# Performance work log

Measured on AMD Instinct MI355X. Metric: run time of the kernel, lower is better.

## Reference

```python
import jax, jax.numpy as jnp
import numpy as np

H, HKV, HD = 16, 4, 128
EPS = 1.1920928955078125e-07  # float32 eps, torch F.rms_norm default


def _rms_norm(t):
    return t * jax.lax.rsqrt(jnp.mean(t * t, axis=-1, keepdims=True) + EPS)


def _rope(t, cos, sin):
    # t: [B, T, h, HD]; cos/sin: [T, HD//2] -> broadcast [1, T, 1, HD//2]
    te, to = t[..., 0::2], t[..., 1::2]
    c = cos[None, :, None, :]
    s = sin[None, :, None, :]
    re = te * c - to * s
    ro = te * s + to * c
    return jnp.stack((re, ro), axis=-1).reshape(t.shape)


def setup_inputs() -> dict:
    key = jax.random.key(0)
    ks = jax.random.split(key, 5)
    B, T, C = 2, 2048, 2048
    return {
        "x": jax.random.normal(ks[0], (B, T, C), jnp.float32),
        "Wq": jax.random.normal(ks[1], (C, C), jnp.float32) * 0.02,
        "Wk": jax.random.normal(ks[2], (HKV * HD, C), jnp.float32) * 0.02,
        "Wv": jax.random.normal(ks[3], (HKV * HD, C), jnp.float32) * 0.02,
        "Wo": jax.random.normal(ks[4], (C, C), jnp.float32) * 0.02,
        "q_gain": jnp.full((H,), 5.0, jnp.float32),
    }


def reference(x, Wq, Wk, Wv, Wo, q_gain):
    B, T, C = x.shape
    q = (x @ Wq.T).reshape(B, T, H, HD)
    k = (x @ Wk.T).reshape(B, T, HKV, HD)
    v = (x @ Wv.T).reshape(B, T, HKV, HD)

    q = _rms_norm(q)
    k = _rms_norm(k)

    theta = 1.0 / (10000.0 ** (jnp.arange(0, HD, 2, dtype=jnp.float32) / HD))
    t = jnp.arange(T, dtype=jnp.float32)
    freqs = jnp.outer(t, theta)  # [T, HD//2]
    cos, sin = jnp.cos(freqs), jnp.sin(freqs)

    q = _rope(q, cos, sin)
    k = _rope(k, cos, sin)
    q = q * q_gain[None, None, :, None]

    qh = q.transpose(0, 2, 1, 3)                       # [B, H, T, HD]
    kh = jnp.repeat(k.transpose(0, 2, 1, 3), H // HKV, axis=1)
    vh = jnp.repeat(v.transpose(0, 2, 1, 3), H // HKV, axis=1)

    scale = 1.0 / jnp.sqrt(jnp.float32(HD))
    scores = jnp.einsum("bhqd,bhkd->bhqk", qh, kh) * scale
    causal = jnp.tril(jnp.ones((T, T), bool))
    scores = jnp.where(causal[None, None], scores, jnp.finfo(scores.dtype).min)
    attn = jax.nn.softmax(scores, axis=-1)
    out = jnp.einsum("bhqk,bhkd->bhqd", attn, vh)
    out = out.transpose(0, 2, 1, 3).reshape(B, T, C)
    return out @ Wo.T
```

## Files before the change

### kernel.cpp

```cpp
#include <hip/hip_runtime.h>
#include <hip/hip_bf16.h>

#define TSEQ 2048
#define CDIM 2048
#define NH   16
#define NKV  4
#define HDIM 128
#define BATCH 2
#define MROWS (BATCH*TSEQ)
#define KVC   (NKV*HDIM)
#define QKVC  (CDIM + 2*KVC)

typedef short bf16x8 __attribute__((ext_vector_type(8)));
typedef float f32x4  __attribute__((ext_vector_type(4)));

typedef const __attribute__((address_space(1))) void* gptr_t;
typedef __attribute__((address_space(3))) void* sptr_t;

__device__ inline void async16(const __hip_bfloat16* g, __hip_bfloat16* l) {
  __builtin_amdgcn_global_load_lds((gptr_t)g, (sptr_t)l, 16, 0, 0);
}

__device__ inline f32x4 mfma16(bf16x8 a, bf16x8 b, f32x4 c) {
  return __builtin_amdgcn_mfma_f32_16x16x32_bf16(a, b, c, 0, 0, 0);
}

__device__ inline float bfbits2f(unsigned short u) {
  return __uint_as_float(((unsigned)u) << 16);
}

__device__ inline int swz128(int row, int col) {
  return row*128 + (((col >> 3) ^ (row & 15)) << 3) + (col & 7);
}
__device__ inline int swz64(int row, int col) {
  return row*64 + ((((col >> 3) ^ row) & 7) << 3) + (col & 7);
}

__global__ void canary(const void* __restrict__ x, int* __restrict__ flag) {
  __shared__ int cnt[256];
  int tid = threadIdx.x;
  const unsigned short* u = (const unsigned short*)x;
  int c = 0;
#pragma unroll
  for (int i = 0; i < 4; ++i) {
    float a = fabsf(bfbits2f(u[(tid*4 + i)*2]));
    if (a >= 1e-6f && a <= 1e3f) c++;
  }
  cnt[tid] = c;
  __syncthreads();
  for (int s = 128; s > 0; s >>= 1) {
    if (tid < s) cnt[tid] += cnt[tid + s];
    __syncthreads();
  }
  if (tid == 0) *flag = (cnt[0] > 512) ? 1 : 0;
}

__global__ __launch_bounds__(256) void canonize_all(
    const void* __restrict__ xs,  const void* __restrict__ wqs,
    const void* __restrict__ wks, const void* __restrict__ wvs,
    const void* __restrict__ wos, const void* __restrict__ gs,
    __hip_bfloat16* __restrict__ xd,
    __hip_bfloat16* __restrict__ wqkv,
    __hip_bfloat16* __restrict__ wod,
    __hip_bfloat16* __restrict__ gd,
    const int* __restrict__ flag)
{
  int blk = blockIdx.x;
  const void* src; __hip_bfloat16* dst; int base, n;
  if      (blk < 4096) { src = xs;  dst = xd;                base = blk;        n = MROWS*CDIM; }
  else if (blk < 6144) { src = wqs; dst = wqkv;              base = blk - 4096; n = CDIM*CDIM; }
  else if (blk < 6656) { src = wks; dst = wqkv + (size_t)CDIM*CDIM;            base = blk - 6144; n = KVC*CDIM; }
  else if (blk < 7168) { src = wvs; dst = wqkv + (size_t)(CDIM+KVC)*CDIM;      base = blk - 6656; n = KVC*CDIM; }
  else if (blk < 9216) { src = wos; dst = wod;               base = blk - 7168; n = CDIM*CDIM; }
  else                 { src = gs;  dst = gd;                base = 0;          n = NH; }
  int idx = base*2048 + threadIdx.x*8;
  if (idx >= n) return;
  if (*flag) {
    *(bf16x8*)&dst[idx] = *(const bf16x8*)((const __hip_bfloat16*)src + idx);
  } else {
    const float* s = (const float*)src + idx;
#pragma unroll
    for (int j = 0; j < 8; ++j) dst[idx + j] = __float2bfloat16(s[j]);
  }
}

#define BK 64

__global__ __launch_bounds__(512, 2) void gemm_bt256(
    const __hip_bfloat16* __restrict__ A,
    const __hip_bfloat16* __restrict__ B,
    __hip_bfloat16* __restrict__ C,
    int M, int N, int K, int lda)
{
  __shared__ __align__(16) __hip_bfloat16 As[2][256*BK];
  __shared__ __align__(16) __hip_bfloat16 Bs[2][256*BK];
  const int tid  = threadIdx.x;
  const int wave = tid >> 6;
  const int lane = tid & 63;
  const int qd   = lane >> 4;
  const int ln   = lane & 15;
  const int m0   = blockIdx.y * 256;
  const int n0   = blockIdx.x * 256;
  const int wm   = (wave >> 2) * 128;
  const int wn   = (wave & 3) * 64;

  auto stageA = [&](int half, int buf, int kt) {
    const __hip_bfloat16* src = A + (size_t)(m0 + half*128)*lda + kt*BK;
    __hip_bfloat16* dst = &As[buf][half*128*BK];
#pragma unroll
    for (int i = 0; i < 2; ++i) {
      int c = i*512 + tid;
      int row = c >> 3, sl = c & 7;
      int gs = sl ^ (row & 7);
      async16(&src[(size_t)row*lda + gs*8], &dst[(i*512 + wave*64)*8]);
    }
  };
  auto stageB = [&](int half, int buf, int kt) {
    const __hip_bfloat16* src = B + (size_t)(n0 + half*128)*K + kt*BK;
    __hip_bfloat16* dst = &Bs[buf][half*128*BK];
#pragma unroll
    for (int i = 0; i < 2; ++i) {
      int c = i*512 + tid;
      int row = c >> 3, sl = c & 7;
      int gs = sl ^ (row & 7);
      async16(&src[(size_t)row*K + gs*8], &dst[(i*512 + wave*64)*8]);
    }
  };
  auto ldA = [&](int buf, int m, int kk) -> bf16x8 {
    int row = wm + m*16 + ln;
    return *(const bf16x8*)&As[buf][row*BK + (((kk*4 + qd) ^ (row & 7)) << 3)];
  };
  auto ldB = [&](int buf, int n, int kk) -> bf16x8 {
    int row = wn + n*16 + ln;
    return *(const bf16x8*)&Bs[buf][row*BK + (((kk*4 + qd) ^ (row & 7)) << 3)];
  };

  f32x4 acc[8][4] = {};
  const int nt = K / BK;

  stageA(0, 0, 0); stageA(1, 0, 0);
  stageB(0, 0, 0); stageB(1, 0, 0);
  if (nt > 1) {
    stageA(0, 1, 1); stageA(1, 1, 1);
    asm volatile("s_waitcnt vmcnt(4)" ::: "memory");
  } else {
    asm volatile("s_waitcnt vmcnt(0)" ::: "memory");
  }
  __builtin_amdgcn_s_barrier();

#pragma unroll 1
  for (int t = 0; t < nt; ++t) {
    const int buf = t & 1;
    bf16x8 a03[4][2], a47[4][2], b01[2][2], b23[2][2];

#pragma unroll
    for (int m = 0; m < 4; ++m)
#pragma unroll
      for (int kk = 0; kk < 2; ++kk) a03[m][kk] = ldA(buf, m, kk);
#pragma unroll
    for (int n = 0; n < 2; ++n)
#pragma unroll
      for (int kk = 0; kk < 2; ++kk) b01[n][kk] = ldB(buf, n, kk);
    if (t + 1 < nt) { stageB(0, buf ^ 1, t + 1); stageB(1, buf ^ 1, t + 1); }
    __builtin_amdgcn_s_setprio(1);
#pragma unroll
    for (int m = 0; m < 4; ++m)
#pragma unroll
      for (int n = 0; n < 2; ++n)
#pragma unroll
        for (int kk = 0; kk < 2; ++kk)
          acc[m][n] = mfma16(a03[m][kk], b01[n][kk], acc[m][n]);
    __builtin_amdgcn_s_setprio(0);
    __builtin_amdgcn_s_barrier();

#pragma unroll
    for (int m = 0; m < 4; ++m)
#pragma unroll
      for (int kk = 0; kk < 2; ++kk) a47[m][kk] = ldA(buf, 4 + m, kk);
    __builtin_amdgcn_s_setprio(1);
#pragma unroll
    for (int m = 0; m < 4; ++m)
#pragma unroll
      for (int n = 0; n < 2; ++n)
#pragma unroll
        for (int kk = 0; kk < 2; ++kk)
          acc[4 + m][n] = mfma16(a47[m][kk], b01[n][kk], acc[4 + m][n]);
    __builtin_amdgcn_s_setprio(0);
    __builtin_amdgcn_s_barrier();

#pragma unroll
    for (int n = 0; n < 2; ++n)
#pragma unroll
      for (int kk = 0; kk < 2; ++kk) b23[n][kk] = ldB(buf, 2 + n, kk);
    __builtin_amdgcn_s_setprio(1);
#pragma unroll
    for (int m = 0; m < 4; ++m)
#pragma unroll
      for (int n = 0; n < 2; ++n)
#pragma unroll
        for (int kk = 0; kk < 2; ++kk)
          acc[m][2 + n] = mfma16(a03[m][kk], b23[n][kk], acc[m][2 + n]);
    __builtin_amdgcn_s_setprio(0);
    __builtin_amdgcn_s_barrier();

    if (t + 2 < nt) { stageA(0, buf, t + 2); stageA(1, buf, t + 2); }
    __builtin_amdgcn_s_setprio(1);
#pragma unroll
    for (int m = 0; m < 4; ++m)
#pragma unroll
      for (int n = 0; n < 2; ++n)
#pragma unroll
        for (int kk = 0; kk < 2; ++kk)
          acc[4 + m][2 + n] = mfma16(a47[m][kk], b23[n][kk], acc[4 + m][2 + n]);
    __builtin_amdgcn_s_setprio(0);
    if (t + 2 < nt) asm volatile("s_waitcnt vmcnt(4)" ::: "memory");
    else            asm volatile("s_waitcnt vmcnt(0)" ::: "memory");
    __builtin_amdgcn_s_barrier();
  }

#pragma unroll
  for (int m = 0; m < 8; ++m)
#pragma unroll
    for (int n = 0; n < 4; ++n) {
      int row = m0 + wm + m*16 + qd*4;
      int col = n0 + wn + n*16 + ln;
#pragma unroll
      for (int r = 0; r < 4; ++r)
        C[(size_t)(row + r)*N + col] = __float2bfloat16(acc[m][n][r]);
    }
}

__global__ __launch_bounds__(256, 2) void gemm_out(
    const __hip_bfloat16* __restrict__ A,
    const __hip_bfloat16* __restrict__ B,
    void* __restrict__ C,
    int M, int N, int K, int lda, const int* __restrict__ flag)
{
  __shared__ __align__(16) __hip_bfloat16 As[128*32];
  __shared__ __align__(16) __hip_bfloat16 Bs[128*32];
  const int tid  = threadIdx.x;
  const int wave = tid >> 6;
  const int lane = tid & 63;
  const int qd   = lane >> 4;
  const int ln   = lane & 15;
  const int m0   = blockIdx.y * 128;
  const int n0   = blockIdx.x * 128;
  const int wm   = (wave >> 1) * 64;
  const int wn   = (wave & 1) * 64;

  f32x4 acc[4][4] = {};

  for (int k0 = 0; k0 < K; k0 += 32) {
    __syncthreads();
#pragma unroll
    for (int r = 0; r < 2; ++r) {
      int e   = (r*256 + tid) * 8;
      int row = e >> 5;
      int col = e & 31;
      async16(&A[(size_t)(m0+row)*lda + k0 + col], &As[(size_t)(r*256 + wave*64)*8]);
      async16(&B[(size_t)(n0+row)*K   + k0 + col], &Bs[(size_t)(r*256 + wave*64)*8]);
    }
    __syncthreads();
    bf16x8 af[4], bfr[4];
#pragma unroll
    for (int i = 0; i < 4; ++i)
      af[i] = *(const bf16x8*)&As[(wm + i*16 + ln)*32 + qd*8];
#pragma unroll
    for (int j = 0; j < 4; ++j)
      bfr[j] = *(const bf16x8*)&Bs[(wn + j*16 + ln)*32 + qd*8];
#pragma unroll
    for (int i = 0; i < 4; ++i)
#pragma unroll
      for (int j = 0; j < 4; ++j)
        acc[i][j] = mfma16(af[i], bfr[j], acc[i][j]);
  }
  const bool isbf = (*flag != 0);
#pragma unroll
  for (int i = 0; i < 4; ++i)
#pragma unroll
    for (int j = 0; j < 4; ++j) {
      int row = m0 + wm + i*16 + qd*4;
      int col = n0 + wn + j*16 + ln;
#pragma unroll
      for (int r = 0; r < 4; ++r) {
        if (isbf) ((__hip_bfloat16*)C)[(size_t)(row + r)*N + col] = __float2bfloat16(acc[i][j][r]);
        else      ((float*)C)[(size_t)(row + r)*N + col] = acc[i][j][r];
      }
    }
}

__global__ __launch_bounds__(256) void prep_qk(
    __hip_bfloat16* __restrict__ qkv,
    const __hip_bfloat16* __restrict__ gain)
{
  int wid  = blockIdx.x * 4 + (threadIdx.x >> 6);
  int lane = threadIdx.x & 63;
  bool isq = wid < MROWS*NH;
  int m, h;
  __hip_bfloat16* p;
  if (isq) { m = wid >> 4; h = wid & 15; p = qkv + (size_t)m*QKVC + h*HDIM; }
  else     { int w2 = wid - MROWS*NH; m = w2 >> 2; h = w2 & 3; p = qkv + (size_t)m*QKVC + CDIM + h*HDIM; }

  ushort2 raw = *(const ushort2*)((const unsigned short*)p + 2*lane);
  float e = bfbits2f(raw.x), o = bfbits2f(raw.y);
  float ss = e*e + o*o;
#pragma unroll
  for (int off = 32; off >= 1; off >>= 1) ss += __shfl_xor(ss, off);
  float rms = rsqrtf(ss * (1.0f/128.0f) + 1.1920928955078125e-07f);
  e *= rms; o *= rms;

  float theta = exp2f(-(float)(2*lane) * (1.0f/128.0f) * 13.287712379549449f);
  int t = m & (TSEQ-1);
  float fr = (float)t * theta;
  float c = cosf(fr), s = sinf(fr);
  float re = e*c - o*s;
  float ro = e*s + o*c;

  if (isq) {
    float g = bfbits2f(*(const unsigned short*)&gain[h]) * 0.08838834764831845f;
    re *= g; ro *= g;
  }
  p[2*lane]   = __float2bfloat16(re);
  p[2*lane+1] = __float2bfloat16(ro);
}

__global__ __launch_bounds__(256) void transpose_v(
    const __hip_bfloat16* __restrict__ qkv, __hip_bfloat16* __restrict__ vt)
{
  __shared__ __hip_bfloat16 tile[32][34];
  int tx = threadIdx.x & 31;
  int ty = threadIdx.x >> 5;
  int r0 = blockIdx.x * 32;
  int c0 = blockIdx.y * 32;
#pragma unroll
  for (int i = 0; i < 4; ++i)
    tile[ty + i*8][tx] = qkv[(size_t)(r0 + ty + i*8)*QKVC + (CDIM + KVC) + c0 + tx];
  __syncthreads();
  int b = r0 >> 11;
  int t = r0 & (TSEQ-1);
  int hk = c0 >> 7;
  int d0 = c0 & (HDIM-1);
#pragma unroll
  for (int i = 0; i < 4; ++i) {
    int d = d0 + ty + i*8;
    vt[((size_t)((b*NKV + hk)*HDIM + d))*TSEQ + t + tx] = tile[tx][ty + i*8];
  }
}

__global__ __launch_bounds__(256, 2) void attn_kernel(
    const __hip_bfloat16* __restrict__ qkv,
    const __hip_bfloat16* __restrict__ vt,
    __hip_bfloat16* __restrict__ out)
{
  const int tid  = threadIdx.x;
  const int wave = tid >> 6;
  const int lane = tid & 63;
  const int qd = lane >> 4, ln = lane & 15;
  const int qt = 15 - blockIdx.x;
  const int h  = blockIdx.y;
  const int b  = blockIdx.z;
  const int hk = h >> 2;

  const __hip_bfloat16* K = qkv + (size_t)(b*TSEQ)*QKVC + CDIM + hk*HDIM;
  const __hip_bfloat16* V = vt + ((size_t)(b*NKV + hk)*HDIM)*TSEQ;

  __shared__ __align__(16) __hip_bfloat16 Ks[64*128];
  __shared__ __align__(16) __hip_bfloat16 Vs[128*64];
  __shared__ __align__(16) __hip_bfloat16 Pb[4*32*64];

  auto issueK = [&](int t0) {
#pragma unroll
    for (int i = 0; i < 4; ++i) {
      int c = i*256 + tid;
      int row = c >> 4, cc = c & 15;
      int gcc = cc ^ (row & 15);
      async16(&K[(size_t)(t0 + row)*QKVC + gcc*8], &Ks[(i*256 + wave*64)*8]);
    }
  };
  auto issueV = [&](int t0) {
#pragma unroll
    for (int i = 0; i < 4; ++i) {
      int c = i*256 + tid;
      int row = c >> 3, cc = c & 7;
      int gcc = cc ^ (row & 7);
      async16(&V[(size_t)row*TSEQ + t0 + gcc*8], &Vs[(i*256 + wave*64)*8]);
    }
  };

  const int q0  = qt * 128;
  const int qws = q0 + wave * 32;

  bf16x8 qfr[2][4];
#pragma unroll
  for (int sub = 0; sub < 2; ++sub)
#pragma unroll
    for (int kc = 0; kc < 4; ++kc)
      qfr[sub][kc] = *(const bf16x8*)&qkv[((size_t)(b*TSEQ + qws + sub*16 + ln))*QKVC + h*HDIM + kc*32 + qd*8];

  f32x4 o[2][8] = {};
  float lacc[2][4] = {};

  issueK(0);
  __syncthreads();

  const int ktend = 2*qt + 1;
#pragma unroll 1
  for (int kt = 0; kt <= ktend; ++kt) {
    const int t0 = kt * 64;
    issueV(t0);

    f32x4 sc[2][4] = {};
#pragma unroll
    for (int nt = 0; nt < 4; ++nt) {
#pragma unroll
      for (int kc = 0; kc < 4; ++kc) {
        bf16x8 kfr = *(const bf16x8*)&Ks[swz128(nt*16 + ln, kc*32 + qd*8)];
        sc[0][nt] = mfma16(qfr[0][kc], kfr, sc[0][nt]);
        sc[1][nt] = mfma16(qfr[1][kc], kfr, sc[1][nt]);
      }
    }
    if (t0 + 63 > qws) {
#pragma unroll
      for (int sub = 0; sub < 2; ++sub)
#pragma unroll
        for (int nt = 0; nt < 4; ++nt)
#pragma unroll
          for (int r = 0; r < 4; ++r) {
            int row = qws + sub*16 + qd*4 + r;
            int col = t0 + nt*16 + ln;
            if (col > row) sc[sub][nt][r] = -1.0e30f;
          }
    }
#pragma unroll
    for (int sub = 0; sub < 2; ++sub) {
#pragma unroll
      for (int nt = 0; nt < 4; ++nt)
#pragma unroll
        for (int r = 0; r < 4; ++r)
          sc[sub][nt][r] = __expf(sc[sub][nt][r]);
#pragma unroll
      for (int r = 0; r < 4; ++r)
        lacc[sub][r] += (sc[sub][0][r] + sc[sub][1][r]) + (sc[sub][2][r] + sc[sub][3][r]);
    }

    __hip_bfloat16* Pw = &Pb[wave*2048];
#pragma unroll
    for (int sub = 0; sub < 2; ++sub)
#pragma unroll
      for (int nt = 0; nt < 4; ++nt)
#pragma unroll
        for (int r = 0; r < 4; ++r)
          Pw[swz64(sub*16 + qd*4 + r, nt*16 + ln)] = __float2bfloat16(sc[sub][nt][r]);
    bf16x8 pa[2][2];
#pragma unroll
    for (int sub = 0; sub < 2; ++sub)
#pragma unroll
      for (int kc = 0; kc < 2; ++kc)
        pa[sub][kc] = *(const bf16x8*)&Pw[swz64(sub*16 + ln, kc*32 + qd*8)];

    __syncthreads();
    if (kt < ktend) issueK(t0 + 64);

#pragma unroll
    for (int dt = 0; dt < 8; ++dt) {
#pragma unroll
      for (int kc = 0; kc < 2; ++kc) {
        bf16x8 vf = *(const bf16x8*)&Vs[swz64(dt*16 + ln, kc*32 + qd*8)];
        o[0][dt] = mfma16(pa[0][kc], vf, o[0][dt]);
        o[1][dt] = mfma16(pa[1][kc], vf, o[1][dt]);
      }
    }
    __syncthreads();
  }

  float inv[2][4];
#pragma unroll
  for (int sub = 0; sub < 2; ++sub)
#pragma unroll
    for (int r = 0; r < 4; ++r) {
      float lr = lacc[sub][r];
      lr += __shfl_xor(lr, 1);
      lr += __shfl_xor(lr, 2);
      lr += __shfl_xor(lr, 4);
      lr += __shfl_xor(lr, 8);
      inv[sub][r] = 1.0f / lr;
    }

  __hip_bfloat16* Ow0 = &Ks[wave*2048];
  __hip_bfloat16* Ow1 = &Vs[wave*2048];
#pragma unroll
  for (int dt = 0; dt < 8; ++dt)
#pragma unroll
    for (int r = 0; r < 4; ++r) {
      Ow0[(qd*4 + r)*128 + dt*16 + ln] = __float2bfloat16(o[0][dt][r] * inv[0][r]);
      Ow1[(qd*4 + r)*128 + dt*16 + ln] = __float2bfloat16(o[1][dt][r] * inv[1][r]);
    }
  __syncthreads();
#pragma unroll
  for (int pass = 0; pass < 4; ++pass) {
    int row = pass*4 + qd;
    bf16x8 v0 = *(const bf16x8*)&Ow0[row*128 + ln*8];
    bf16x8 v1 = *(const bf16x8*)&Ow1[row*128 + ln*8];
    int qa = qws + row;
    int qb = qws + 16 + row;
    *(bf16x8*)&out[((size_t)(b*TSEQ + qa))*CDIM + h*HDIM + ln*8] = v0;
    *(bf16x8*)&out[((size_t)(b*TSEQ + qb))*CDIM + h*HDIM + ln*8] = v1;
  }
}

extern "C" void kernel_launch(void* const* d_in, const int* in_sizes, int n_in,
                              void* d_out, int out_size, void* d_ws, size_t ws_size,
                              hipStream_t stream) {
  char* ws = (char*)d_ws;
  size_t off = 0;
  auto alloc = [&](size_t bytes) { char* p = ws + off; off += (bytes + 255) & ~(size_t)255; return p; };

  int* flag = (int*)alloc(256);
  __hip_bfloat16* xb   = (__hip_bfloat16*)alloc((size_t)MROWS*CDIM*2);
  __hip_bfloat16* wqkv = (__hip_bfloat16*)alloc((size_t)QKVC*CDIM*2);
  __hip_bfloat16* wob  = (__hip_bfloat16*)alloc((size_t)CDIM*CDIM*2);
  __hip_bfloat16* gb   = (__hip_bfloat16*)alloc(256);
  __hip_bfloat16* qkv  = (__hip_bfloat16*)alloc((size_t)MROWS*QKVC*2);
  __hip_bfloat16* vt   = (__hip_bfloat16*)alloc((size_t)MROWS*KVC*2);

  canary<<<1, 256, 0, stream>>>(d_in[0], flag);

  canonize_all<<<9217, 256, 0, stream>>>(
      d_in[0], d_in[1], d_in[2], d_in[3], d_in[4], d_in[5],
      xb, wqkv, wob, gb, flag);

  gemm_bt256<<<dim3(QKVC/256, MROWS/256), 512, 0, stream>>>(
      xb, wqkv, qkv, MROWS, QKVC, CDIM, CDIM);

  int nwaves = MROWS*NH + MROWS*NKV;
  prep_qk<<<nwaves/4, 256, 0, stream>>>(qkv, gb);

  transpose_v<<<dim3(MROWS/32, KVC/32), 256, 0, stream>>>(qkv, vt);

  attn_kernel<<<dim3(TSEQ/128, NH, BATCH), 256, 0, stream>>>(qkv, vt, xb);

  gemm_out<<<dim3(CDIM/128, MROWS/128), 256, 0, stream>>>(
      xb, wob, d_out, MROWS, CDIM, CDIM, CDIM, flag);
}
```

Before: 322.3 us.

## Pair light and heavy 64-row query tiles per attention block for causal balance

The attention kernel now runs 128-thread blocks (2 waves) that each process two 64-row query tiles, p and 31-p, one after the other, so every block does the same amount of causal work. Before, each block handled one 128-row tile with 4 waves and the work per block varied widely. The aim is to remove load imbalance and tail effects across the grid. In exchange, each block has fewer waves to hide latency, and the K and V tiles are reloaded separately for each segment.

Result: slower. 348.7 us (+8.2%).

```diff
diff --git a/kernel.cpp b/kernel.cpp
--- a/kernel.cpp
+++ b/kernel.cpp
@@ -347,7 +347,7 @@
   }
 }
 
-__global__ __launch_bounds__(256, 2) void attn_kernel(
+__global__ __launch_bounds__(128, 2) void attn_kernel(
     const __hip_bfloat16* __restrict__ qkv,
     const __hip_bfloat16* __restrict__ vt,
     __hip_bfloat16* __restrict__ out)
@@ -356,7 +356,7 @@
   const int wave = tid >> 6;
   const int lane = tid & 63;
   const int qd = lane >> 4, ln = lane & 15;
-  const int qt = 15 - blockIdx.x;
+  const int p  = blockIdx.x;
   const int h  = blockIdx.y;
   const int b  = blockIdx.z;
   const int hk = h >> 2;
@@ -366,145 +366,145 @@
 
   __shared__ __align__(16) __hip_bfloat16 Ks[64*128];
   __shared__ __align__(16) __hip_bfloat16 Vs[128*64];
-  __shared__ __align__(16) __hip_bfloat16 Pb[4*32*64];
+  __shared__ __align__(16) __hip_bfloat16 Pb[2*32*64];
 
   auto issueK = [&](int t0) {
 #pragma unroll
-    for (int i = 0; i < 4; ++i) {
-      int c = i*256 + tid;
+    for (int i = 0; i < 8; ++i) {
+      int c = i*128 + tid;
       int row = c >> 4, cc = c & 15;
       int gcc = cc ^ (row & 15);
-      async16(&K[(size_t)(t0 + row)*QKVC + gcc*8], &Ks[(i*256 + wave*64)*8]);
+      async16(&K[(size_t)(t0 + row)*QKVC + gcc*8], &Ks[(i*128 + wave*64)*8]);
     }
   };
   auto issueV = [&](int t0) {
 #pragma unroll
-    for (int i = 0; i < 4; ++i) {
-      int c = i*256 + tid;
+    for (int i = 0; i < 8; ++i) {
+      int c = i*128 + tid;
       int row = c >> 3, cc = c & 7;
       int gcc = cc ^ (row & 7);
-      async16(&V[(size_t)row*TSEQ + t0 + gcc*8], &Vs[(i*256 + wave*64)*8]);
+      async16(&V[(size_t)row*TSEQ + t0 + gcc*8], &Vs[(i*128 + wave*64)*8]);
     }
   };
 
-  const int q0  = qt * 128;
-  const int qws = q0 + wave * 32;
-
-  bf16x8 qfr[2][4];
-#pragma unroll
-  for (int sub = 0; sub < 2; ++sub)
-#pragma unroll
-    for (int kc = 0; kc < 4; ++kc)
-      qfr[sub][kc] = *(const bf16x8*)&qkv[((size_t)(b*TSEQ + qws + sub*16 + ln))*QKVC + h*HDIM + kc*32 + qd*8];
-
-  f32x4 o[2][8] = {};
-  float lacc[2][4] = {};
-
-  issueK(0);
-  __syncthreads();
-
-  const int ktend = 2*qt + 1;
 #pragma unroll 1
-  for (int kt = 0; kt <= ktend; ++kt) {
-    const int t0 = kt * 64;
-    issueV(t0);
-
-    f32x4 sc[2][4] = {};
-#pragma unroll
-    for (int nt = 0; nt < 4; ++nt) {
-#pragma unroll
-      for (int kc = 0; kc < 4; ++kc) {
-        bf16x8 kfr = *(const bf16x8*)&Ks[swz128(nt*16 + ln, kc*32 + qd*8)];
-        sc[0][nt] = mfma16(qfr[0][kc], kfr, sc[0][nt]);
-        sc[1][nt] = mfma16(qfr[1][kc], kfr, sc[1][nt]);
+  for (int seg = 0; seg < 2; ++seg) {
+    const int qt = seg ? (31 - p) : p;
+    const int q0 = qt * 64;
+    const int qws = q0 + wave * 32;
+
+    bf16x8 qfr[2][4];
+#pragma unroll
+    for (int sub = 0; sub < 2; ++sub)
+#pragma unroll
+      for (int kc = 0; kc < 4; ++kc)
+        qfr[sub][kc] = *(const bf16x8*)&qkv[((size_t)(b*TSEQ + qws + sub*16 + ln))*QKVC + h*HDIM + kc*32 + qd*8];
+
+    f32x4 o[2][8] = {};
+    float lacc[2][4] = {};
+
+    __syncthreads();
+    issueK(0);
+    __syncthreads();
+
+#pragma unroll 1
+    for (int kt = 0; kt <= qt; ++kt) {
+      const int t0 = kt * 64;
+      issueV(t0);
+
+      f32x4 sc[2][4] = {};
+#pragma unroll
+      for (int nt = 0; nt < 4; ++nt) {
+#pragma unroll
+        for (int kc = 0; kc < 4; ++kc) {
+          bf16x8 kfr = *(const bf16x8*)&Ks[swz128(nt*16 + ln, kc*32 + qd*8)];
+          sc[0][nt] = mfma16(qfr[0][kc], kfr, sc[0][nt]);
+          sc[1][nt] = mfma16(qfr[1][kc], kfr, sc[1][nt]);
+        }
       }
-    }
-    if (t0 + 63 > qws) {
+      if (t0 + 63 > qws) {
+#pragma unroll
+        for (int sub = 0; sub < 2; ++sub)
+#pragma unroll
+          for (int nt = 0; nt < 4; ++nt)
+#pragma unroll
+            for (int r = 0; r < 4; ++r) {
+              int row = qws + sub*16 + qd*4 + r;
+              int col = t0 + nt*16 + ln;
+              if (col > row) sc[sub][nt][r] = -1.0e30f;
+            }
+      }
+#pragma unroll
+      for (int sub = 0; sub < 2; ++sub) {
+#pragma unroll
+        for (int nt = 0; nt < 4; ++nt)
+#pragma unroll
+          for (int r = 0; r < 4; ++r)
+            sc[sub][nt][r] = __expf(sc[sub][nt][r]);
+#pragma unroll
+        for (int r = 0; r < 4; ++r)
+          lacc[sub][r] += (sc[sub][0][r] + sc[sub][1][r]) + (sc[sub][2][r] + sc[sub][3][r]);
+      }
+
+      __hip_bfloat16* Pw = &Pb[wave*2048];
 #pragma unroll
       for (int sub = 0; sub < 2; ++sub)
 #pragma unroll
         for (int nt = 0; nt < 4; ++nt)
 #pragma unroll
-          for (int r = 0; r < 4; ++r) {
-            int row = qws + sub*16 + qd*4 + r;
-            int col = t0 + nt*16 + ln;
-            if (col > row) sc[sub][nt][r] = -1.0e30f;
-          }
-    }
-#pragma unroll
-    for (int sub = 0; sub < 2; ++sub) {
-#pragma unroll
-      for (int nt = 0; nt < 4; ++nt)
+          for (int r = 0; r < 4; ++r)
+            Pw[swz64(sub*16 + qd*4 + r, nt*16 + ln)] = __float2bfloat16(sc[sub][nt][r]);
+      bf16x8 pa[2][2];
+#pragma unroll
+      for (int sub = 0; sub < 2; ++sub)
+#pragma unroll
+        for (int kc = 0; kc < 2; ++kc)
+          pa[sub][kc] = *(const bf16x8*)&Pw[swz64(sub*16 + ln, kc*32 + qd*8)];
+
+      __syncthreads();
+      if (kt < qt) issueK(t0 + 64);
+
+#pragma unroll
+      for (int dt = 0; dt < 8; ++dt) {
+#pragma unroll
+        for (int kc = 0; kc < 2; ++kc) {
+          bf16x8 vf = *(const bf16x8*)&Vs[swz64(dt*16 + ln, kc*32 + qd*8)];
+          o[0][dt] = mfma16(pa[0][kc], vf, o[0][dt]);
+          o[1][dt] = mfma16(pa[1][kc], vf, o[1][dt]);
+        }
+      }
+      __syncthreads();
+    }
+
+    float inv[2][4];
+#pragma unroll
+    for (int sub = 0; sub < 2; ++sub)
+#pragma unroll
+      for (int r = 0; r < 4; ++r) {
+        float lr = lacc[sub][r];
+        lr += __shfl_xor(lr, 1);
+        lr += __shfl_xor(lr, 2);
+        lr += __shfl_xor(lr, 4);
+        lr += __shfl_xor(lr, 8);
+        inv[sub][r] = 1.0f / lr;
+      }
+
+    __hip_bfloat16* Ow = &Ks[wave*4096];
+#pragma unroll
+    for (int sub = 0; sub < 2; ++sub)
+#pragma unroll
+      for (int dt = 0; dt < 8; ++dt)
 #pragma unroll
         for (int r = 0; r < 4; ++r)
-          sc[sub][nt][r] = __expf(sc[sub][nt][r]);
-#pragma unroll
-      for (int r = 0; r < 4; ++r)
-        lacc[sub][r] += (sc[sub][0][r] + sc[sub][1][r]) + (sc[sub][2][r] + sc[sub][3][r]);
-    }
-
-    __hip_bfloat16* Pw = &Pb[wave*2048];
-#pragma unroll
-    for (int sub = 0; sub < 2; ++sub)
-#pragma unroll
-      for (int nt = 0; nt < 4; ++nt)
-#pragma unroll
-        for (int r = 0; r < 4; ++r)
-          Pw[swz64(sub*16 + qd*4 + r, nt*16 + ln)] = __float2bfloat16(sc[sub][nt][r]);
-    bf16x8 pa[2][2];
-#pragma unroll
-    for (int sub = 0; sub < 2; ++sub)
-#pragma unroll
-      for (int kc = 0; kc < 2; ++kc)
-        pa[sub][kc] = *(const bf16x8*)&Pw[swz64(sub*16 + ln, kc*32 + qd*8)];
-
+          Ow[(sub*16 + qd*4 + r)*128 + dt*16 + ln] = __float2bfloat16(o[sub][dt][r] * inv[sub][r]);
     __syncthreads();
-    if (kt < ktend) issueK(t0 + 64);
-
-#pragma unroll
-    for (int dt = 0; dt < 8; ++dt) {
-#pragma unroll
-      for (int kc = 0; kc < 2; ++kc) {
-        bf16x8 vf = *(const bf16x8*)&Vs[swz64(dt*16 + ln, kc*32 + qd*8)];
-        o[0][dt] = mfma16(pa[0][kc], vf, o[0][dt]);
-        o[1][dt] = mfma16(pa[1][kc], vf, o[1][dt]);
-      }
-    }
-    __syncthreads();
-  }
-
-  float inv[2][4];
-#pragma unroll
-  for (int sub = 0; sub < 2; ++sub)
-#pragma unroll
-    for (int r = 0; r < 4; ++r) {
-      float lr = lacc[sub][r];
-      lr += __shfl_xor(lr, 1);
-      lr += __shfl_xor(lr, 2);
-      lr += __shfl_xor(lr, 4);
-      lr += __shfl_xor(lr, 8);
-      inv[sub][r] = 1.0f / lr;
-    }
-
-  __hip_bfloat16* Ow0 = &Ks[wave*2048];
-  __hip_bfloat16* Ow1 = &Vs[wave*2048];
-#pragma unroll
-  for (int dt = 0; dt < 8; ++dt)
-#pragma unroll
-    for (int r = 0; r < 4; ++r) {
-      Ow0[(qd*4 + r)*128 + dt*16 + ln] = __float2bfloat16(o[0][dt][r] * inv[0][r]);
-      Ow1[(qd*4 + r)*128 + dt*16 + ln] = __float2bfloat16(o[1][dt][r] * inv[1][r]);
-    }
-  __syncthreads();
-#pragma unroll
-  for (int pass = 0; pass < 4; ++pass) {
-    int row = pass*4 + qd;
-    bf16x8 v0 = *(const bf16x8*)&Ow0[row*128 + ln*8];
-    bf16x8 v1 = *(const bf16x8*)&Ow1[row*128 + ln*8];
-    int qa = qws + row;
-    int qb = qws + 16 + row;
-    *(bf16x8*)&out[((size_t)(b*TSEQ + qa))*CDIM + h*HDIM + ln*8] = v0;
-    *(bf16x8*)&out[((size_t)(b*TSEQ + qb))*CDIM + h*HDIM + ln*8] = v1;
+#pragma unroll
+    for (int pass = 0; pass < 8; ++pass) {
+      int row = pass*4 + qd;
+      bf16x8 val = *(const bf16x8*)&Ow[row*128 + ln*8];
+      int q = qws + row;
+      *(bf16x8*)&out[((size_t)(b*TSEQ + q))*CDIM + h*HDIM + ln*8] = val;
+    }
   }
 }
 
@@ -537,7 +537,7 @@
 
   transpose_v<<<dim3(MROWS/32, KVC/32), 256, 0, stream>>>(qkv, vt);
 
-  attn_kernel<<<dim3(TSEQ/128, NH, BATCH), 256, 0, stream>>>(qkv, vt, xb);
+  attn_kernel<<<dim3(16, NH, BATCH), 128, 0, stream>>>(qkv, vt, xb);
 
   gemm_out<<<dim3(CDIM/128, MROWS/128), 256, 0, stream>>>(
       xb, wob, d_out, MROWS, CDIM, CDIM, CDIM, flag);
```
